# Optimization experiments

Hardware: AMD Instinct MI355X
Metric: run time of the kernel (lower is better)

The kernel has to match this reference:

```python
import jax, jax.numpy as jnp
import numpy as np

B, S, D, H = 2, 2048, 1024, 16
HD = D // H  # head_dim = 64


def setup_inputs() -> dict:
    key = jax.random.key(0)
    ks = jax.random.split(key, 10)
    sc = 1.0 / np.sqrt(D)
    x = jax.random.normal(ks[0], (B, S, D), dtype=jnp.float32)
    # causal mask, 0 = masked (module does masked_fill(mask == 0, -1e9))
    mask = jnp.broadcast_to(jnp.tril(jnp.ones((S, S), dtype=jnp.int32)), (B, S, S))
    return {
        "x": x,
        "mask": mask,
        "Wq": jax.random.normal(ks[1], (D, D), dtype=jnp.float32) * sc,
        "bq": jnp.zeros((D,), dtype=jnp.float32),
        "Wk": jax.random.normal(ks[2], (D, D), dtype=jnp.float32) * sc,
        "bk": jnp.zeros((D,), dtype=jnp.float32),
        "Wv": jax.random.normal(ks[3], (D, D), dtype=jnp.float32) * sc,
        "bv": jnp.zeros((D,), dtype=jnp.float32),
        "Wo": jax.random.normal(ks[4], (D, D), dtype=jnp.float32) * sc,
        "bo": jnp.zeros((D,), dtype=jnp.float32),
    }


def reference(x, mask, Wq, bq, Wk, bk, Wv, bv, Wo, bo):
    b, s, _ = x.shape
    # torch nn.Linear: y = x @ W.T + b
    def split_heads(t):
        return t.reshape(b, s, H, HD).transpose(0, 2, 1, 3)  # [B,H,S,hd]
    q = split_heads(x @ Wq.T + bq)
    k = split_heads(x @ Wk.T + bk)
    v = split_heads(x @ Wv.T + bv)
    scores = jnp.einsum("bhqd,bhkd->bhqk", q, k) / jnp.sqrt(jnp.float32(HD))
    scores = jnp.where(mask[:, None, :, :] == 0, jnp.float32(-1e9), scores)
    w = jax.nn.softmax(scores, axis=-1)
    out = jnp.einsum("bhqk,bhkd->bhqd", w, v)  # [B,H,S,hd]
    out = out.transpose(0, 2, 1, 3).reshape(b, s, D)
    return out @ Wo.T + bo
```

## Files before the change

kernel.cpp:

```cpp
#include <hip/hip_runtime.h>
#include <cstdint>


typedef __bf16 bf16x8 __attribute__((ext_vector_type(8)));
typedef float f32x4 __attribute__((ext_vector_type(4)));

__device__ inline f32x4 mfma16(bf16x8 a, bf16x8 b, f32x4 c) {
    return __builtin_amdgcn_mfma_f32_16x16x32_bf16(a, b, c, 0, 0, 0);
}

__device__ inline uint16_t f2bf(float f) {
    uint32_t u = __builtin_bit_cast(uint32_t, f);
    u += 0x7FFFu + ((u >> 16) & 1u);
    return (uint16_t)(u >> 16);
}

__device__ inline void gload_lds16(const uint16_t* g, uint16_t* l) {
    __builtin_amdgcn_global_load_lds(
        (const __attribute__((address_space(1))) uint32_t*)g,
        (__attribute__((address_space(3))) uint32_t*)l, 16, 0, 0);
}

__global__ __launch_bounds__(256) void cast_all(const float* __restrict__ x,
                                                const float* __restrict__ wq,
                                                const float* __restrict__ wk,
                                                const float* __restrict__ wv,
                                                const float* __restrict__ wo,
                                                uint16_t* __restrict__ xbf,
                                                uint16_t* __restrict__ wbf) {
    int i = blockIdx.x * 256 + threadIdx.x;
    float4 v;
    uint64_t* dp;
    if (i < (1 << 20)) {
        v = ((const float4*)x)[i];
        dp = (uint64_t*)xbf + i;
    } else {
        int j = i - (1 << 20);
        const float* ws[4] = {wq, wk, wv, wo};
        v = ((const float4*)ws[j >> 18])[j & 0x3FFFF];
        dp = (uint64_t*)wbf + j;
    }
    uint64_t p = (uint64_t)f2bf(v.x) | ((uint64_t)f2bf(v.y) << 16) |
                 ((uint64_t)f2bf(v.z) << 32) | ((uint64_t)f2bf(v.w) << 48);
    *dp = p;
}

template<int OUTF32, int BN>
__global__ __launch_bounds__(256) void gemm128(const uint16_t* __restrict__ A,
                                               const uint16_t* __restrict__ W,
                                               const float* __restrict__ b0,
                                               const float* __restrict__ b1,
                                               const float* __restrict__ b2,
                                               void* __restrict__ o0,
                                               void* __restrict__ o1,
                                               void* __restrict__ o2,
                                               int K, float s0, float s1, float s2) {
    constexpr int NT = BN / 32;
    __shared__ __align__(16) uint16_t SH[2 * (128 + BN) * 32];
    const int tid = threadIdx.x;
    const int lane = tid & 63, w = tid >> 6;
    const int l16 = lane & 15, quad = lane >> 4;
    const int wm = w & 1, wn = w >> 1;
    const int m0 = blockIdx.x * 128, n0 = blockIdx.y * BN;

    f32x4 acc[4][NT] = {};

    const int ci0 = w * 128 + lane;
    const uint16_t* ga0 = A + (size_t)(m0 + (ci0 >> 2)) * K + (ci0 & 3) * 8;
    const int ci1 = ci0 + 64;
    const uint16_t* ga1 = A + (size_t)(m0 + (ci1 >> 2)) * K + (ci1 & 3) * 8;
    const uint16_t* gb0 = W + (size_t)(n0 + (ci0 >> 2)) * K + (ci0 & 3) * 8;
    const uint16_t* gb1 = W + (size_t)(n0 + (ci1 >> 2)) * K + (ci1 & 3) * 8;
    const uint16_t* gbS = W + (size_t)(n0 + (tid >> 2)) * K + (tid & 3) * 8;

    uint16_t* A0 = SH;
    uint16_t* B0 = SH + 128 * 32;
    uint16_t* A1 = SH + (128 + BN) * 32;
    uint16_t* B1 = A1 + 128 * 32;

    gload_lds16(ga0, A0 + (w * 2 + 0) * 512);
    gload_lds16(ga1, A0 + (w * 2 + 1) * 512);
    if constexpr (BN == 128) {
        gload_lds16(gb0, B0 + (w * 2 + 0) * 512);
        gload_lds16(gb1, B0 + (w * 2 + 1) * 512);
    } else {
        gload_lds16(gbS, B0 + w * 512);
    }

    const int niter = K >> 5;
    for (int i = 0; i < niter; ++i) {
        __syncthreads();
        if (i + 1 < niter) {
            const int k1 = (i + 1) << 5;
            uint16_t* Ad = (i & 1) ? A0 : A1;
            uint16_t* Bd = (i & 1) ? B0 : B1;
            gload_lds16(ga0 + k1, Ad + (w * 2 + 0) * 512);
            gload_lds16(ga1 + k1, Ad + (w * 2 + 1) * 512);
            if constexpr (BN == 128) {
                gload_lds16(gb0 + k1, Bd + (w * 2 + 0) * 512);
                gload_lds16(gb1 + k1, Bd + (w * 2 + 1) * 512);
            } else {
                gload_lds16(gbS + k1, Bd + w * 512);
            }
        }
        const uint16_t* Ab = (i & 1) ? A1 : A0;
        const uint16_t* Bb = (i & 1) ? B1 : B0;
        bf16x8 af[4], bw[NT];
#pragma unroll
        for (int t = 0; t < 4; ++t)
            af[t] = *(const bf16x8*)(Ab + (wm * 64 + t * 16 + l16) * 32 + quad * 8);
#pragma unroll
        for (int t = 0; t < NT; ++t)
            bw[t] = *(const bf16x8*)(Bb + (wn * (BN / 2) + t * 16 + l16) * 32 + quad * 8);
#pragma unroll
        for (int mt = 0; mt < 4; ++mt)
#pragma unroll
            for (int nt = 0; nt < NT; ++nt)
                acc[mt][nt] = mfma16(af[mt], bw[nt], acc[mt][nt]);
    }

    const int seg = n0 >> 10, lc0 = n0 & 1023;
    const float* bp = (seg == 0) ? b0 : (seg == 1 ? b1 : b2);
    const float scale = (seg == 0) ? s0 : (seg == 1 ? s1 : s2);
    void* op = (seg == 0) ? o0 : (seg == 1 ? o1 : o2);

    if constexpr (OUTF32) {
#pragma unroll
        for (int nt = 0; nt < NT; ++nt) {
            int lcol = lc0 + wn * (BN / 2) + nt * 16 + l16;
            float bc = bp[lcol];
#pragma unroll
            for (int mt = 0; mt < 4; ++mt)
#pragma unroll
                for (int r = 0; r < 4; ++r) {
                    int row = m0 + wm * 64 + mt * 16 + quad * 4 + r;
                    ((float*)op)[(size_t)row * 1024 + lcol] = (acc[mt][nt][r] + bc) * scale;
                }
        }
    } else {
        __syncthreads();
        uint16_t* EP = SH;
#pragma unroll
        for (int nt = 0; nt < NT; ++nt) {
            float bc = bp[lc0 + wn * (BN / 2) + nt * 16 + l16];
#pragma unroll
            for (int mt = 0; mt < 4; ++mt)
#pragma unroll
                for (int r = 0; r < 4; ++r)
                    EP[(wm * 64 + mt * 16 + quad * 4 + r) * 128 +
                       wn * (BN / 2) + nt * 16 + l16] =
                        f2bf((acc[mt][nt][r] + bc) * scale);
        }
        __syncthreads();
        if (seg == 2) {
            const int bb = m0 >> 11, s0v = m0 & 2047;
            const int h0 = (n0 - 2048) >> 6;
            uint16_t* vtb = (uint16_t*)op + ((size_t)(bb * 16 + h0) * 64) * 2048 + s0v;
#pragma unroll
            for (int it = 0; it < 8; ++it) {
                int id = it * 256 + tid;
                int c = id & 127, sg = id >> 7;
                uint32_t wpk[4];
#pragma unroll
                for (int jj = 0; jj < 4; ++jj) {
                    uint32_t lo = EP[(sg * 8 + 2 * jj) * 128 + c];
                    uint32_t hi = EP[(sg * 8 + 2 * jj + 1) * 128 + c];
                    wpk[jj] = lo | (hi << 16);
                }
                uint4 o; o.x = wpk[0]; o.y = wpk[1]; o.z = wpk[2]; o.w = wpk[3];
                *(uint4*)(vtb + (size_t)c * 2048 + sg * 8) = o;
            }
        } else {
#pragma unroll
            for (int p = 0; p < 8; ++p) {
                int row = p * 16 + (tid >> 4);
                int c8 = (tid & 15) * 8;
                uint4 v = *(const uint4*)(EP + row * 128 + c8);
                *(uint4*)((uint16_t*)op + (size_t)(m0 + row) * 1024 + lc0 + c8) = v;
            }
        }
    }
}

__global__ __launch_bounds__(256) void attn_kernel(const uint16_t* __restrict__ Q,
                                                   const uint16_t* __restrict__ K,
                                                   const uint16_t* __restrict__ Vt,
                                                   uint16_t* __restrict__ att) {
    const int S = 2048, D = 1024;
    constexpr int LD = 72;
    __shared__ __align__(16) uint16_t Klds[2][64 * LD];
    __shared__ __align__(16) uint16_t Vlds[2][64 * LD];
    __shared__ __align__(16) uint16_t Plds[4 * 32 * LD];

    const int bh = blockIdx.y;
    const int qb = (bh & 16) ? (int)blockIdx.x : 15 - (int)blockIdx.x;
    const int niter = 2 * qb + 2, kb_diag = 2 * qb;

    const int b = bh >> 4, h = bh & 15;
    const int tid = threadIdx.x, lane = tid & 63, w = tid >> 6;
    const int l16 = lane & 15, quad = lane >> 4;
    const int q0 = qb * 128;
    const size_t baseQK = (size_t)b * S * D + h * 64;
    uint16_t* Pw = Plds + w * (32 * LD);

    bf16x8 aq[2][2];
#pragma unroll
    for (int mt = 0; mt < 2; ++mt)
#pragma unroll
        for (int c = 0; c < 2; ++c)
            aq[mt][c] = *(const bf16x8*)(Q + baseQK +
                (size_t)(q0 + w * 32 + mt * 16 + l16) * D + c * 32 + quad * 8);

    bf16x8 ones;
#pragma unroll
    for (int j = 0; j < 8; ++j) ones[j] = (__bf16)1.0f;

    f32x4 accO[2][4] = {};
    f32x4 accL[2] = {};

    const int srow = tid >> 2, scq = tid & 3;
    const uint16_t* Kg = K + baseQK + (size_t)srow * D + scq * 16;
    const uint16_t* Vg = Vt + ((size_t)bh * 64 + srow) * S + scq * 16;
    const int soff = srow * LD + scq * 16;

    uint4 kA, kB, vA, vB;
    kA = *(const uint4*)Kg; kB = *(const uint4*)(Kg + 8);
    vA = *(const uint4*)Vg; vB = *(const uint4*)(Vg + 8);
    *(uint4*)(Klds[0] + soff)     = kA;
    *(uint4*)(Klds[0] + soff + 8) = kB;
    *(uint4*)(Vlds[0] + soff)     = vA;
    *(uint4*)(Vlds[0] + soff + 8) = vB;
    {
        const uint16_t* kg = Kg + (size_t)64 * D;
        const uint16_t* vg = Vg + 64;
        kA = *(const uint4*)kg; kB = *(const uint4*)(kg + 8);
        vA = *(const uint4*)vg; vB = *(const uint4*)(vg + 8);
    }
    __syncthreads();

    for (int kb = 0; kb < niter; ++kb) {
        const uint16_t* Kb = Klds[kb & 1];
        const uint16_t* Vb = Vlds[kb & 1];

        if (kb + 1 < niter) {
            uint16_t* Kd = (uint16_t*)Klds[(kb + 1) & 1];
            uint16_t* Vd = (uint16_t*)Vlds[(kb + 1) & 1];
            *(uint4*)(Kd + soff)     = kA;
            *(uint4*)(Kd + soff + 8) = kB;
            *(uint4*)(Vd + soff)     = vA;
            *(uint4*)(Vd + soff + 8) = vB;
            if (kb + 2 < niter) {
                const uint16_t* kg = Kg + (size_t)((kb + 2) * 64) * D;
                const uint16_t* vg = Vg + (kb + 2) * 64;
                kA = *(const uint4*)kg; kB = *(const uint4*)(kg + 8);
                vA = *(const uint4*)vg; vB = *(const uint4*)(vg + 8);
            }
        }

        f32x4 sc[2][4];
#pragma unroll
        for (int t = 0; t < 4; ++t) {
            bf16x8 bk0 = *(const bf16x8*)(Kb + (t * 16 + l16) * LD + quad * 8);
            bf16x8 bk1 = *(const bf16x8*)(Kb + (t * 16 + l16) * LD + 32 + quad * 8);
            f32x4 z0 = {}; f32x4 z1 = {};
            sc[0][t] = mfma16(bk1, aq[0][1], mfma16(bk0, aq[0][0], z0));
            sc[1][t] = mfma16(bk1, aq[1][1], mfma16(bk0, aq[1][0], z1));
        }

        bf16x8 bv0[4], bv1[4];
#pragma unroll
        for (int nt = 0; nt < 4; ++nt) {
            bv0[nt] = *(const bf16x8*)(Vb + (nt * 16 + l16) * LD + quad * 8);
            bv1[nt] = *(const bf16x8*)(Vb + (nt * 16 + l16) * LD + 32 + quad * 8);
        }

        if (kb < kb_diag) {
#pragma unroll
            for (int mt = 0; mt < 2; ++mt) {
                uint16_t* prow = Pw + (mt * 16 + l16) * LD + quad * 4;
#pragma unroll
                for (int t = 0; t < 4; ++t) {
                    uint64_t pk = 0;
#pragma unroll
                    for (int r = 0; r < 4; ++r) {
                        float p = __builtin_amdgcn_exp2f(sc[mt][t][r]);
                        pk |= (uint64_t)(uint16_t)(__builtin_bit_cast(uint32_t, p) >> 16)
                              << (16 * r);
                    }
                    *(uint64_t*)(prow + t * 16) = pk;
                }
            }
        } else {
#pragma unroll
            for (int mt = 0; mt < 2; ++mt) {
                const int qrow = q0 + w * 32 + mt * 16 + l16;
                uint16_t* prow = Pw + (mt * 16 + l16) * LD + quad * 4;
#pragma unroll
                for (int t = 0; t < 4; ++t) {
                    const int kc0 = kb * 64 + t * 16 + quad * 4;
                    uint64_t pk = 0;
#pragma unroll
                    for (int r = 0; r < 4; ++r) {
                        float s = sc[mt][t][r];
                        if (kc0 + r > qrow) s = -1e30f;
                        float p = __builtin_amdgcn_exp2f(s);
                        pk |= (uint64_t)(uint16_t)(__builtin_bit_cast(uint32_t, p) >> 16)
                              << (16 * r);
                    }
                    *(uint64_t*)(prow + t * 16) = pk;
                }
            }
        }

        __asm__ volatile("s_waitcnt lgkmcnt(0)" ::: "memory");

        bf16x8 ap0[2], ap1[2];
#pragma unroll
        for (int mt = 0; mt < 2; ++mt) {
            ap0[mt] = *(const bf16x8*)(Pw + (mt * 16 + l16) * LD + quad * 8);
            ap1[mt] = *(const bf16x8*)(Pw + (mt * 16 + l16) * LD + 32 + quad * 8);
        }
#pragma unroll
        for (int nt = 0; nt < 4; ++nt) {
            accO[0][nt] = mfma16(ap1[0], bv1[nt], mfma16(ap0[0], bv0[nt], accO[0][nt]));
            accO[1][nt] = mfma16(ap1[1], bv1[nt], mfma16(ap0[1], bv0[nt], accO[1][nt]));
        }
        accL[0] = mfma16(ap1[0], ones, mfma16(ap0[0], ones, accL[0]));
        accL[1] = mfma16(ap1[1], ones, mfma16(ap0[1], ones, accL[1]));

        if (kb + 1 < niter) __syncthreads();
    }

    __asm__ volatile("s_waitcnt lgkmcnt(0)" ::: "memory");
#pragma unroll
    for (int mt = 0; mt < 2; ++mt)
#pragma unroll
        for (int r = 0; r < 4; ++r) {
            float inv = __builtin_amdgcn_rcpf(accL[mt][r]);
            const int rl = mt * 16 + quad * 4 + r;
#pragma unroll
            for (int nt = 0; nt < 4; ++nt)
                Pw[rl * LD + nt * 16 + l16] = f2bf(accO[mt][nt][r] * inv);
        }
    __asm__ volatile("s_waitcnt lgkmcnt(0)" ::: "memory");
#pragma unroll
    for (int p = 0; p < 4; ++p) {
        int row = p * 8 + (lane >> 3);
        int c8 = (lane & 7) * 8;
        uint4 v = *(const uint4*)(Pw + row * LD + c8);
        *(uint4*)(att + (size_t)(b * S + q0 + w * 32 + row) * 1024 + h * 64 + c8) = v;
    }
}

extern "C" void kernel_launch(void* const* d_in, const int* in_sizes, int n_in,
                              void* d_out, int out_size, void* d_ws, size_t ws_size,
                              hipStream_t stream) {
    const float* x  = (const float*)d_in[0];
    const float* Wq = (const float*)d_in[2];
    const float* bq = (const float*)d_in[3];
    const float* Wk = (const float*)d_in[4];
    const float* bk = (const float*)d_in[5];
    const float* Wv = (const float*)d_in[6];
    const float* bv = (const float*)d_in[7];
    const float* Wo = (const float*)d_in[8];
    const float* bo = (const float*)d_in[9];
    float* out = (float*)d_out;

    const int B = 2, S = 2048, D = 1024, H = 16;
    const int M = B * S;

    uint8_t* w = (uint8_t*)d_ws;
    uint16_t* xbf  = (uint16_t*)(w);
    uint16_t* wqbf = (uint16_t*)(w + (size_t)( 8 << 20));
    uint16_t* qbf  = (uint16_t*)(w + (size_t)(16 << 20));
    uint16_t* kbf  = (uint16_t*)(w + (size_t)(24 << 20));
    uint16_t* vtbf = (uint16_t*)(w + (size_t)(40 << 20));
    uint16_t* wobf = wqbf + (size_t)3 * D * D;
    uint16_t* attbf = xbf;

    cast_all<<<dim3((1 << 21) / 256), dim3(256), 0, stream>>>(
        x, Wq, Wk, Wv, Wo, xbf, wqbf);

    gemm128<0, 128><<<dim3(M / 128, 3072 / 128), dim3(256), 0, stream>>>(
        xbf, wqbf, bq, bk, bv, qbf, kbf, vtbf, D, 0.125f * 1.44269504f, 1.0f, 1.0f);

    attn_kernel<<<dim3(16, B * H), dim3(256), 0, stream>>>(qbf, kbf, vtbf, attbf);

    gemm128<1, 64><<<dim3(M / 128, 1024 / 64), dim3(256), 0, stream>>>(
        attbf, wobf, bo, bo, bo, out, out, out, D, 1.0f, 1.0f, 1.0f);
}
```

Measured before the change: 196.7 us.

## Load K/V fragments directly from global memory, dropping LDS staging and barriers

The attention kernel no longer stages K and V tiles in double-buffered shared memory. Each wave now loads its MFMA operand fragments straight from global memory, relying on L1/L2 to serve the loads repeated across the four waves. This removes the shared-memory round trip, the register prefetch and the per-iteration block barrier, and frees LDS for occupancy. In exchange, every wave issues its own global loads with no software prefetch, so the MFMAs may stall on memory latency and cache traffic rises.

Measured after the change: 229.2 us. +16.5%, slower.

```diff
diff --git a/kernel.cpp b/kernel.cpp
--- a/kernel.cpp
+++ b/kernel.cpp
@@ -188,8 +188,6 @@
                                                    uint16_t* __restrict__ att) {
     const int S = 2048, D = 1024;
     constexpr int LD = 72;
-    __shared__ __align__(16) uint16_t Klds[2][64 * LD];
-    __shared__ __align__(16) uint16_t Vlds[2][64 * LD];
     __shared__ __align__(16) uint16_t Plds[4 * 32 * LD];
 
     const int bh = blockIdx.y;
@@ -218,60 +216,32 @@
     f32x4 accO[2][4] = {};
     f32x4 accL[2] = {};
 
-    const int srow = tid >> 2, scq = tid & 3;
-    const uint16_t* Kg = K + baseQK + (size_t)srow * D + scq * 16;
-    const uint16_t* Vg = Vt + ((size_t)bh * 64 + srow) * S + scq * 16;
-    const int soff = srow * LD + scq * 16;
-
-    uint4 kA, kB, vA, vB;
-    kA = *(const uint4*)Kg; kB = *(const uint4*)(Kg + 8);
-    vA = *(const uint4*)Vg; vB = *(const uint4*)(Vg + 8);
-    *(uint4*)(Klds[0] + soff)     = kA;
-    *(uint4*)(Klds[0] + soff + 8) = kB;
-    *(uint4*)(Vlds[0] + soff)     = vA;
-    *(uint4*)(Vlds[0] + soff + 8) = vB;
-    {
-        const uint16_t* kg = Kg + (size_t)64 * D;
-        const uint16_t* vg = Vg + 64;
-        kA = *(const uint4*)kg; kB = *(const uint4*)(kg + 8);
-        vA = *(const uint4*)vg; vB = *(const uint4*)(vg + 8);
-    }
-    __syncthreads();
+    const uint16_t* Kf = K + baseQK + (size_t)l16 * D + quad * 8;
+    const uint16_t* Vf = Vt + ((size_t)bh * 64 + l16) * S + quad * 8;
 
     for (int kb = 0; kb < niter; ++kb) {
-        const uint16_t* Kb = Klds[kb & 1];
-        const uint16_t* Vb = Vlds[kb & 1];
-
-        if (kb + 1 < niter) {
-            uint16_t* Kd = (uint16_t*)Klds[(kb + 1) & 1];
-            uint16_t* Vd = (uint16_t*)Vlds[(kb + 1) & 1];
-            *(uint4*)(Kd + soff)     = kA;
-            *(uint4*)(Kd + soff + 8) = kB;
-            *(uint4*)(Vd + soff)     = vA;
-            *(uint4*)(Vd + soff + 8) = vB;
-            if (kb + 2 < niter) {
-                const uint16_t* kg = Kg + (size_t)((kb + 2) * 64) * D;
-                const uint16_t* vg = Vg + (kb + 2) * 64;
-                kA = *(const uint4*)kg; kB = *(const uint4*)(kg + 8);
-                vA = *(const uint4*)vg; vB = *(const uint4*)(vg + 8);
-            }
+        const uint16_t* Kt = Kf + (size_t)(kb * 64) * D;
+        bf16x8 k0[4], k1[4];
+#pragma unroll
+        for (int t = 0; t < 4; ++t) {
+            k0[t] = *(const bf16x8*)(Kt + (size_t)(t * 16) * D);
+            k1[t] = *(const bf16x8*)(Kt + (size_t)(t * 16) * D + 32);
         }
 
         f32x4 sc[2][4];
 #pragma unroll
         for (int t = 0; t < 4; ++t) {
-            bf16x8 bk0 = *(const bf16x8*)(Kb + (t * 16 + l16) * LD + quad * 8);
-            bf16x8 bk1 = *(const bf16x8*)(Kb + (t * 16 + l16) * LD + 32 + quad * 8);
             f32x4 z0 = {}; f32x4 z1 = {};
-            sc[0][t] = mfma16(bk1, aq[0][1], mfma16(bk0, aq[0][0], z0));
-            sc[1][t] = mfma16(bk1, aq[1][1], mfma16(bk0, aq[1][0], z1));
-        }
-
+            sc[0][t] = mfma16(k1[t], aq[0][1], mfma16(k0[t], aq[0][0], z0));
+            sc[1][t] = mfma16(k1[t], aq[1][1], mfma16(k0[t], aq[1][0], z1));
+        }
+
+        const uint16_t* Vtt = Vf + kb * 64;
         bf16x8 bv0[4], bv1[4];
 #pragma unroll
         for (int nt = 0; nt < 4; ++nt) {
-            bv0[nt] = *(const bf16x8*)(Vb + (nt * 16 + l16) * LD + quad * 8);
-            bv1[nt] = *(const bf16x8*)(Vb + (nt * 16 + l16) * LD + 32 + quad * 8);
+            bv0[nt] = *(const bf16x8*)(Vtt + (size_t)(nt * 16) * S);
+            bv1[nt] = *(const bf16x8*)(Vtt + (size_t)(nt * 16) * S + 32);
         }
 
         if (kb < kb_diag) {
@@ -327,8 +297,6 @@
         }
         accL[0] = mfma16(ap1[0], ones, mfma16(ap0[0], ones, accL[0]));
         accL[1] = mfma16(ap1[1], ones, mfma16(ap0[1], ones, accL[1]));
-
-        if (kb + 1 < niter) __syncthreads();
     }
 
     __asm__ volatile("s_waitcnt lgkmcnt(0)" ::: "memory");
```
